# Optimization experiments

Hardware: AMD Instinct MI355X
Metric: run time of the kernel (lower is better)

## Reference

```python
import jax, jax.numpy as jnp
import numpy as np

N_NODES = 128   # input_series_dim (nodes per graph)
FEAT = 512      # input_series_length
HID = 512       # hidden_channels
OUT = 10        # output_dimension
BATCH = 512     # batch_size


def setup_inputs() -> dict:
    key = jax.random.key(0)
    ks = jax.random.split(key, 9)
    s = 0.02
    x = jax.random.normal(ks[0], (BATCH, N_NODES, FEAT), jnp.float32)
    # dense_to_sparse(ones(N_NODES, N_NODES)) -> fully connected incl. diagonal,
    # row-major order, covering only nodes 0..N_NODES-1 (faithful to source).
    r = jnp.repeat(jnp.arange(N_NODES, dtype=jnp.int32), N_NODES)
    c = jnp.tile(jnp.arange(N_NODES, dtype=jnp.int32), N_NODES)
    edge_index = jnp.stack([r, c])  # (2, N_NODES**2)
    batch = jnp.repeat(jnp.arange(BATCH, dtype=jnp.int32), N_NODES)  # (BATCH*N_NODES,)
    W1 = jax.random.normal(ks[1], (FEAT, HID), jnp.float32) * s
    b1 = jnp.zeros((HID,), jnp.float32)
    W2 = jax.random.normal(ks[2], (HID, HID), jnp.float32) * s
    b2 = jnp.zeros((HID,), jnp.float32)
    W3 = jax.random.normal(ks[3], (HID, HID), jnp.float32) * s
    b3 = jnp.zeros((HID,), jnp.float32)
    Wlin = jax.random.normal(ks[4], (HID, OUT), jnp.float32) * s
    blin = jnp.zeros((OUT,), jnp.float32)
    return {"x": x, "W1": W1, "b1": b1, "W2": W2, "b2": b2, "W3": W3,
            "b3": b3, "Wlin": Wlin, "blin": blin,
            "edge_index": edge_index, "batch": batch}


def gcn_conv(h, src, dst, W, b):
    # PyG GCNConv: linear transform, add self-loops for ALL N nodes, symmetric norm,
    # scatter-add aggregate at dst, add bias.
    N = h.shape[0]
    h = h @ W
    loop = jnp.arange(N, dtype=src.dtype)
    s = jnp.concatenate([src, loop])
    d = jnp.concatenate([dst, loop])
    deg = jax.ops.segment_sum(jnp.ones(s.shape[0], h.dtype), d, num_segments=N)
    dinv = jnp.where(deg > 0, jax.lax.rsqrt(deg), jnp.zeros((), h.dtype))
    norm = dinv[s] * dinv[d]                     # (E+N,)
    out = jax.ops.segment_sum(norm[:, None] * h[s], d, num_segments=N)
    return out + b


def reference(x, W1, b1, W2, b2, W3, b3, Wlin, blin, edge_index, batch):
    x = x.reshape(-1, x.shape[-1]).astype(jnp.float32)   # (B*N_NODES, FEAT)
    src, dst = edge_index[0], edge_index[1]
    h = jax.nn.relu(gcn_conv(x, src, dst, W1, b1))
    h = jax.nn.relu(gcn_conv(h, src, dst, W2, b2))
    h = gcn_conv(h, src, dst, W3, b3)                    # layers == 3 path
    B = BATCH
    sums = jax.ops.segment_sum(h, batch, num_segments=B)
    cnt = jax.ops.segment_sum(jnp.ones((h.shape[0],), h.dtype), batch, num_segments=B)
    pooled = sums / cnt[:, None]                         # global_mean_pool
    # dropout p=0.5 is identity in eval mode
    return pooled @ Wlin + blin                          # (BATCH, OUT)
```

## Files before the change

kernel.cpp:

```cpp
#include <hip/hip_runtime.h>
#include <hip/hip_bf16.h>


typedef __attribute__((ext_vector_type(8))) short short8;
typedef __attribute__((ext_vector_type(4))) float f32x4;
typedef __attribute__((ext_vector_type(2))) unsigned int uint2v;

#define AS_G __attribute__((address_space(1)))
#define AS_L __attribute__((address_space(3)))

__device__ __forceinline__ void gload_lds16(const void* g, void* l) {
  __builtin_amdgcn_global_load_lds((const AS_G void*)g, (AS_L void*)l, 16, 0, 0);
}

__device__ __forceinline__ unsigned int pack2_bf16(float a, float b) {
  unsigned int ua = __float_as_uint(a);
  unsigned int ub = __float_as_uint(b);
  ua += 0x7FFFu + ((ua >> 16) & 1u);
  ub += 0x7FFFu + ((ub >> 16) & 1u);
  return (ua >> 16) | (ub & 0xFFFF0000u);
}

__device__ __forceinline__ unsigned short bf16_rne(float a) {
  unsigned int ua = __float_as_uint(a);
  ua += 0x7FFFu + ((ua >> 16) & 1u);
  return (unsigned short)(ua >> 16);
}


__global__ __launch_bounds__(1024) void gemm1_f32a(
    const float* __restrict__ A,
    const __hip_bfloat16* __restrict__ Bt,
    const float* __restrict__ bias,
    unsigned short* __restrict__ H,
    float* __restrict__ g0)
{
  __shared__ __align__(16) __hip_bfloat16 smem[40960];

  const int t  = threadIdx.x;
  const int bm = blockIdx.x;
  const int m0 = bm * 128;

  const int wave = t >> 6;
  const int l    = t & 63;
  const int q    = l >> 4;
  const int r16  = l & 15;
  const int wm   = (wave & 1) * 64;
  const int wn   = (wave >> 1) * 64;

  const int brow = t >> 2;
  const int bgc  = (t & 3) ^ ((brow >> 1) & 3);
  const __hip_bfloat16* gb0 = Bt + (size_t)brow * 512 + bgc * 8;
  const __hip_bfloat16* gb1 = gb0 + (size_t)256 * 512;
  __hip_bfloat16* lB0 = smem + wave * 512;
  __hip_bfloat16* lB1 = smem + 8192 + wave * 512;

  const int arow = t >> 3;
  const int kq   = t & 7;
  const float* ga = A + (size_t)(m0 + arow) * 512 + kq * 4;
  const int ac    = (kq >> 1) ^ ((arow >> 1) & 3);
  const int awoff = arow * 32 + ac * 8 + (kq & 1) * 4;

  f32x4 acc[4][4];
#pragma unroll
  for (int i = 0; i < 4; ++i)
#pragma unroll
    for (int j = 0; j < 4; ++j)
      acc[i][j] = (f32x4)0.0f;

  {
    f32x4 a0 = *(const f32x4*)(const void*)ga;
    gload_lds16(gb0, lB0);
    gload_lds16(gb1, lB1);
    uint2v w;
    w[0] = pack2_bf16(a0[0], a0[1]);
    w[1] = pack2_bf16(a0[2], a0[3]);
    *(uint2v*)(void*)(smem + 32768 + awoff) = w;
  }

  for (int kt = 0; kt < 16; ++kt) {
    const int cur = kt & 1;
    const int nxt = cur ^ 1;
    __syncthreads();

    f32x4 aN;
    if (kt < 15) {
      const int ko = (kt + 1) * 32;
      aN = *(const f32x4*)(const void*)(ga + ko);
      gload_lds16(gb0 + ko, smem + nxt * 16384 + wave * 512);
      gload_lds16(gb1 + ko, smem + nxt * 16384 + 8192 + wave * 512);
    }

    short8 af[4], bfr[4];
#pragma unroll
    for (int i = 0; i < 4; ++i) {
      const int row = wm + i * 16 + r16;
      const int c   = (q ^ ((row >> 1) & 3)) << 3;
      af[i] = *(const short8*)(const void*)(smem + 32768 + cur * 4096 + row * 32 + c);
    }
#pragma unroll
    for (int j = 0; j < 4; ++j) {
      const int row = wn + j * 16 + r16;
      const int c   = (q ^ ((row >> 1) & 3)) << 3;
      bfr[j] = *(const short8*)(const void*)(smem + cur * 16384 + row * 32 + c);
    }

#pragma unroll
    for (int i = 0; i < 4; ++i)
#pragma unroll
      for (int j = 0; j < 4; ++j)
        acc[i][j] = __builtin_amdgcn_mfma_f32_16x16x32_bf16(af[i], bfr[j], acc[i][j], 0, 0, 0);

    if (kt < 15) {
      uint2v w;
      w[0] = pack2_bf16(aN[0], aN[1]);
      w[1] = pack2_bf16(aN[2], aN[3]);
      *(uint2v*)(void*)(smem + 32768 + nxt * 4096 + awoff) = w;
    }
  }

  if (bm == 0) {
#pragma unroll
    for (int i = 0; i < 4; ++i)
#pragma unroll
      for (int j = 0; j < 4; ++j) {
        const int col = wn + j * 16 + r16;
#pragma unroll
        for (int r = 0; r < 4; ++r)
          g0[(wm + i * 16 + q * 4 + r) * 512 + col] = acc[i][j][r];
      }
    return;
  }
#pragma unroll
  for (int j = 0; j < 4; ++j) {
    const int col = wn + j * 16 + r16;
    const float bv = bias[col];
#pragma unroll
    for (int i = 0; i < 4; ++i)
#pragma unroll
      for (int r = 0; r < 4; ++r) {
        const int row = m0 + wm + i * 16 + q * 4 + r;
        const float v = fmaxf(acc[i][j][r] + bv, 0.0f);
        const float o = __shfl_xor(v, 1, 64);
        if ((r16 & 1) == 0)
          *(unsigned int*)(void*)(H + (size_t)row * 512 + col) = pack2_bf16(v, o);
      }
  }
}

__global__ __launch_bounds__(1024) void gemm2_pool(
    const __hip_bfloat16* __restrict__ A,
    const __hip_bfloat16* __restrict__ Bt,
    const float* __restrict__ bias,
    float* __restrict__ g0,
    float* __restrict__ P)
{
  __shared__ __align__(16) __hip_bfloat16 smem[40960];

  const int t  = threadIdx.x;
  const int bm = blockIdx.x;
  const int m0 = bm * 128;

  const int wave = t >> 6;
  const int l    = t & 63;
  const int q    = l >> 4;
  const int r16  = l & 15;
  const int wm   = (wave & 1) * 64;
  const int wn   = (wave >> 1) * 64;

  const int brow = t >> 2;
  const int bgc  = (t & 3) ^ ((brow >> 1) & 3);
  const __hip_bfloat16* gb0 = Bt + (size_t)brow * 512 + bgc * 8;
  const __hip_bfloat16* gb1 = gb0 + (size_t)256 * 512;
  __hip_bfloat16* lB0 = smem + wave * 512;
  __hip_bfloat16* lB1 = smem + 8192 + wave * 512;

  const __hip_bfloat16* ga = A + (size_t)(m0 + brow) * 512 + bgc * 8;
  __hip_bfloat16* lA = smem + 32768 + wave * 512;

  f32x4 acc[4][4];
#pragma unroll
  for (int i = 0; i < 4; ++i)
#pragma unroll
    for (int j = 0; j < 4; ++j)
      acc[i][j] = (f32x4)0.0f;

  if (t < 512) gload_lds16(ga, lA);
  gload_lds16(gb0, lB0);
  gload_lds16(gb1, lB1);

  for (int kt = 0; kt < 16; ++kt) {
    const int cur = kt & 1;
    const int nxt = cur ^ 1;
    __syncthreads();

    if (kt < 15) {
      const int ko = (kt + 1) * 32;
      if (t < 512) gload_lds16(ga + ko, smem + 32768 + nxt * 4096 + wave * 512);
      gload_lds16(gb0 + ko, smem + nxt * 16384 + wave * 512);
      gload_lds16(gb1 + ko, smem + nxt * 16384 + 8192 + wave * 512);
    }

    short8 af[4], bfr[4];
#pragma unroll
    for (int i = 0; i < 4; ++i) {
      const int row = wm + i * 16 + r16;
      const int c   = (q ^ ((row >> 1) & 3)) << 3;
      af[i] = *(const short8*)(const void*)(smem + 32768 + cur * 4096 + row * 32 + c);
    }
#pragma unroll
    for (int j = 0; j < 4; ++j) {
      const int row = wn + j * 16 + r16;
      const int c   = (q ^ ((row >> 1) & 3)) << 3;
      bfr[j] = *(const short8*)(const void*)(smem + cur * 16384 + row * 32 + c);
    }

#pragma unroll
    for (int i = 0; i < 4; ++i)
#pragma unroll
      for (int j = 0; j < 4; ++j)
        acc[i][j] = __builtin_amdgcn_mfma_f32_16x16x32_bf16(af[i], bfr[j], acc[i][j], 0, 0, 0);
  }

  __syncthreads();
  float* red = (float*)(smem + 32768);

  if (bm == 0) {
#pragma unroll
    for (int i = 0; i < 4; ++i)
#pragma unroll
      for (int j = 0; j < 4; ++j) {
        const int col = wn + j * 16 + r16;
#pragma unroll
        for (int r = 0; r < 4; ++r)
          g0[(wm + i * 16 + q * 4 + r) * 512 + col] = acc[i][j][r];
      }
    return;
  }

  float s[4];
#pragma unroll
  for (int j = 0; j < 4; ++j) {
    const float bv = bias[wn + j * 16 + r16];
    float a = 0.0f;
#pragma unroll
    for (int i = 0; i < 4; ++i)
#pragma unroll
      for (int r = 0; r < 4; ++r)
        a += fmaxf(acc[i][j][r] + bv, 0.0f);
    a += __shfl_xor(a, 16, 64);
    a += __shfl_xor(a, 32, 64);
    s[j] = a;
  }
  if (q == 0) {
#pragma unroll
    for (int j = 0; j < 4; ++j) red[wave * 64 + j * 16 + r16] = s[j];
  }
  __syncthreads();
  if (t < 512) {
    const int band = t >> 6;
    const int c = t & 63;
    P[(size_t)bm * 512 + band * 64 + c] =
        (red[2 * band * 64 + c] + red[(2 * band + 1) * 64 + c]) * (1.0f / 128.0f);
  }
}

__global__ void fixup_g0_h(const float* __restrict__ g0,
                           const float* __restrict__ bias,
                           unsigned short* __restrict__ H) {
  const int c = blockIdx.x * 128 + threadIdx.x;
  float S = 0.0f;
  for (int i = 0; i < 128; ++i) S += g0[i * 512 + c];
  const float bv = bias[c];
  for (int i = 0; i < 128; ++i) {
    const float v = (S + g0[i * 512 + c]) * (1.0f / 129.0f) + bv;
    H[i * 512 + c] = bf16_rne(fmaxf(v, 0.0f));
  }
}

__global__ void fixup_g0_pool(const float* __restrict__ g0,
                              const float* __restrict__ bias,
                              float* __restrict__ P) {
  const int c = blockIdx.x * 128 + threadIdx.x;
  float S = 0.0f;
  for (int i = 0; i < 128; ++i) S += g0[i * 512 + c];
  const float bv = bias[c];
  float ps = 0.0f;
  for (int i = 0; i < 128; ++i)
    ps += fmaxf((S + g0[i * 512 + c]) * (1.0f / 129.0f) + bv, 0.0f);
  P[c] = ps * (1.0f / 128.0f);
}

__global__ void fold_w(const float* __restrict__ W3,
                       const float* __restrict__ Wlin,
                       const float* __restrict__ b3,
                       const float* __restrict__ blin,
                       float* __restrict__ Wf, float* __restrict__ bfv) {
  const int c = blockIdx.x;
  const int l = threadIdx.x;
  float acc[10];
#pragma unroll
  for (int o = 0; o < 10; ++o) acc[o] = 0.0f;
  for (int n = l; n < 512; n += 64) {
    const float wv = W3[c * 512 + n];
#pragma unroll
    for (int o = 0; o < 10; ++o) acc[o] += wv * Wlin[n * 10 + o];
  }
#pragma unroll
  for (int off = 32; off; off >>= 1)
#pragma unroll
    for (int o = 0; o < 10; ++o) acc[o] += __shfl_down(acc[o], off, 64);
  if (l == 0) {
#pragma unroll
    for (int o = 0; o < 10; ++o) Wf[c * 10 + o] = acc[o];
  }
  if (c < 10) {
    float s = 0.0f;
    for (int k = l; k < 512; k += 64) s += b3[k] * Wlin[k * 10 + c];
#pragma unroll
    for (int off = 32; off; off >>= 1) s += __shfl_down(s, off, 64);
    if (l == 0) bfv[c] = s + blin[c];
  }
}

__global__ void final_out(const float* __restrict__ P,
                          const float* __restrict__ Wf,
                          const float* __restrict__ bfv,
                          float* __restrict__ out) {
  const int m = blockIdx.x;
  const int l = threadIdx.x;
  float acc[10];
#pragma unroll
  for (int o = 0; o < 10; ++o) acc[o] = 0.0f;
  for (int c = l; c < 512; c += 64) {
    const float p = P[m * 512 + c];
#pragma unroll
    for (int o = 0; o < 10; ++o) acc[o] += p * Wf[c * 10 + o];
  }
#pragma unroll
  for (int off = 32; off; off >>= 1)
#pragma unroll
    for (int o = 0; o < 10; ++o) acc[o] += __shfl_down(acc[o], off, 64);
  if (l == 0) {
#pragma unroll
    for (int o = 0; o < 10; ++o) out[m * 10 + o] = acc[o] + bfv[o];
  }
}

__global__ void transpose512x2(const float* __restrict__ Wa,
                               const float* __restrict__ Wb,
                               unsigned short* __restrict__ Wat,
                               unsigned short* __restrict__ Wbt) {
  const float* W = blockIdx.z ? Wb : Wa;
  unsigned short* Wt = blockIdx.z ? Wbt : Wat;
  __shared__ float tile[32][33];
  const int tx = threadIdx.x, ty = threadIdx.y;
  tile[ty][tx] = W[(blockIdx.y * 32 + ty) * 512 + blockIdx.x * 32 + tx];
  __syncthreads();
  Wt[(blockIdx.x * 32 + ty) * 512 + blockIdx.y * 32 + tx] = bf16_rne(tile[tx][ty]);
}

extern "C" void kernel_launch(void* const* d_in, const int* in_sizes, int n_in,
                              void* d_out, int out_size, void* d_ws, size_t ws_size,
                              hipStream_t stream) {
  const float* x    = (const float*)d_in[0];
  const float* W1   = (const float*)d_in[1];
  const float* b1   = (const float*)d_in[2];
  const float* W2   = (const float*)d_in[3];
  const float* b2   = (const float*)d_in[4];
  const float* W3   = (const float*)d_in[5];
  const float* b3   = (const float*)d_in[6];
  const float* Wlin = (const float*)d_in[7];
  const float* blin = (const float*)d_in[8];
  float* out = (float*)d_out;

  char* ws = (char*)d_ws;
  const size_t MB = (size_t)1 << 20;
  unsigned short* H1  = (unsigned short*)ws;
  float* g0           = (float*)(ws + 64 * MB);
  float* P            = (float*)(ws + 64 * MB + 256 * 1024);
  unsigned short* W1t = (unsigned short*)(ws + 65 * MB + 256 * 1024);
  unsigned short* W2t = W1t + 512 * 512;
  float* Wf           = (float*)(W2t + 512 * 512);
  float* bfv          = Wf + 512 * 10;

  transpose512x2<<<dim3(16, 16, 2), dim3(32, 32), 0, stream>>>(W1, W2, W1t, W2t);
  fold_w<<<512, 64, 0, stream>>>(W3, Wlin, b3, blin, Wf, bfv);

  gemm1_f32a<<<512, 1024, 0, stream>>>(
      x, (const __hip_bfloat16*)W1t, b1, H1, g0);
  fixup_g0_h<<<4, 128, 0, stream>>>(g0, b1, H1);

  gemm2_pool<<<512, 1024, 0, stream>>>(
      (const __hip_bfloat16*)H1, (const __hip_bfloat16*)W2t, b2, g0, P);
  fixup_g0_pool<<<4, 128, 0, stream>>>(g0, b2, P);

  final_out<<<512, 64, 0, stream>>>(P, Wf, bfv, out);
}
```

Measured before the change: 331.7 us.

## Fuse both GCN GEMM layers per graph keeping hidden activations in LDS

Merges the first and second GEMM kernels into one kernel per 128-node block. The bf16 hidden activations stay in a swizzled 128x512 LDS tile instead of round-tripping through a global H buffer, and the graph-0 fixups are done in-block via an LDS column reduction, which removes two small fixup launches. This saves about 64 MB of global traffic and two launches. In exchange LDS use doubles to 160 KB, and the second GEMM loads W2 single-buffered with two barriers per k-step, so it loses load/compute overlap.

```diff
diff --git a/kernel.cpp b/kernel.cpp
--- a/kernel.cpp
+++ b/kernel.cpp
@@ -27,20 +27,18 @@
   return (unsigned short)(ua >> 16);
 }
 
-
-__global__ __launch_bounds__(1024) void gemm1_f32a(
-    const float* __restrict__ A,
-    const __hip_bfloat16* __restrict__ Bt,
-    const float* __restrict__ bias,
-    unsigned short* __restrict__ H,
-    float* __restrict__ g0)
+__global__ __launch_bounds__(1024) void fused_gcn(
+    const float* __restrict__ x,
+    const __hip_bfloat16* __restrict__ W1t,
+    const __hip_bfloat16* __restrict__ W2t,
+    const float* __restrict__ b1,
+    const float* __restrict__ b2,
+    float* __restrict__ P)
 {
-  __shared__ __align__(16) __hip_bfloat16 smem[40960];
+  __shared__ __align__(16) __hip_bfloat16 smem[81920];
 
   const int t  = threadIdx.x;
-  const int bm = blockIdx.x;
-  const int m0 = bm * 128;
-
+  const int g  = blockIdx.x;
   const int wave = t >> 6;
   const int l    = t & 63;
   const int q    = l >> 4;
@@ -48,18 +46,16 @@
   const int wm   = (wave & 1) * 64;
   const int wn   = (wave >> 1) * 64;
 
+  const int arow = t >> 3;
+  const int kq   = t & 7;
+  const float* ga = x + ((size_t)g * 128 + arow) * 512 + kq * 4;
+  const int awoff = arow * 32 + (((kq >> 1) ^ ((arow >> 1) & 3)) << 3) + (kq & 1) * 4;
+
   const int brow = t >> 2;
   const int bgc  = (t & 3) ^ ((brow >> 1) & 3);
-  const __hip_bfloat16* gb0 = Bt + (size_t)brow * 512 + bgc * 8;
-  const __hip_bfloat16* gb1 = gb0 + (size_t)256 * 512;
-  __hip_bfloat16* lB0 = smem + wave * 512;
-  __hip_bfloat16* lB1 = smem + 8192 + wave * 512;
-
-  const int arow = t >> 3;
-  const int kq   = t & 7;
-  const float* ga = A + (size_t)(m0 + arow) * 512 + kq * 4;
-  const int ac    = (kq >> 1) ^ ((arow >> 1) & 3);
-  const int awoff = arow * 32 + ac * 8 + (kq & 1) * 4;
+  const size_t boff = (size_t)brow * 512 + bgc * 8;
+  const __hip_bfloat16* g1b0 = W1t + boff;
+  const __hip_bfloat16* g1b1 = g1b0 + (size_t)256 * 512;
 
   f32x4 acc[4][4];
 #pragma unroll
@@ -70,14 +66,13 @@
 
   {
     f32x4 a0 = *(const f32x4*)(const void*)ga;
-    gload_lds16(gb0, lB0);
-    gload_lds16(gb1, lB1);
+    gload_lds16(g1b0, smem + 49152 + wave * 512);
+    gload_lds16(g1b1, smem + 49152 + 8192 + wave * 512);
     uint2v w;
     w[0] = pack2_bf16(a0[0], a0[1]);
     w[1] = pack2_bf16(a0[2], a0[3]);
-    *(uint2v*)(void*)(smem + 32768 + awoff) = w;
-  }
-
+    *(uint2v*)(void*)(smem + awoff) = w;
+  }
   for (int kt = 0; kt < 16; ++kt) {
     const int cur = kt & 1;
     const int nxt = cur ^ 1;
@@ -87,8 +82,8 @@
     if (kt < 15) {
       const int ko = (kt + 1) * 32;
       aN = *(const f32x4*)(const void*)(ga + ko);
-      gload_lds16(gb0 + ko, smem + nxt * 16384 + wave * 512);
-      gload_lds16(gb1 + ko, smem + nxt * 16384 + 8192 + wave * 512);
+      gload_lds16(g1b0 + ko, smem + 49152 + nxt * 16384 + wave * 512);
+      gload_lds16(g1b1 + ko, smem + 49152 + nxt * 16384 + 8192 + wave * 512);
     }
 
     short8 af[4], bfr[4];
@@ -96,15 +91,14 @@
     for (int i = 0; i < 4; ++i) {
       const int row = wm + i * 16 + r16;
       const int c   = (q ^ ((row >> 1) & 3)) << 3;
-      af[i] = *(const short8*)(const void*)(smem + 32768 + cur * 4096 + row * 32 + c);
+      af[i] = *(const short8*)(const void*)(smem + cur * 4096 + row * 32 + c);
     }
 #pragma unroll
     for (int j = 0; j < 4; ++j) {
       const int row = wn + j * 16 + r16;
       const int c   = (q ^ ((row >> 1) & 3)) << 3;
-      bfr[j] = *(const short8*)(const void*)(smem + cur * 16384 + row * 32 + c);
-    }
-
+      bfr[j] = *(const short8*)(const void*)(smem + 49152 + cur * 16384 + row * 32 + c);
+    }
 #pragma unroll
     for (int i = 0; i < 4; ++i)
 #pragma unroll
@@ -115,180 +109,174 @@
       uint2v w;
       w[0] = pack2_bf16(aN[0], aN[1]);
       w[1] = pack2_bf16(aN[2], aN[3]);
-      *(uint2v*)(void*)(smem + 32768 + nxt * 4096 + awoff) = w;
-    }
-  }
-
-  if (bm == 0) {
-#pragma unroll
-    for (int i = 0; i < 4; ++i)
-#pragma unroll
-      for (int j = 0; j < 4; ++j) {
-        const int col = wn + j * 16 + r16;
+      *(uint2v*)(void*)(smem + nxt * 4096 + awoff) = w;
+    }
+  }
+  __syncthreads();
+
+  float* redf = (float*)(smem + 65536);
+  float* Sbuf = (float*)(smem + 67584);
+
+  if (g == 0) {
+    float sj[4];
+#pragma unroll
+    for (int j = 0; j < 4; ++j) {
+      float a = 0.0f;
+#pragma unroll
+      for (int i = 0; i < 4; ++i)
 #pragma unroll
         for (int r = 0; r < 4; ++r)
-          g0[(wm + i * 16 + q * 4 + r) * 512 + col] = acc[i][j][r];
-      }
-    return;
-  }
-#pragma unroll
-  for (int j = 0; j < 4; ++j) {
-    const int col = wn + j * 16 + r16;
-    const float bv = bias[col];
-#pragma unroll
-    for (int i = 0; i < 4; ++i)
-#pragma unroll
-      for (int r = 0; r < 4; ++r) {
-        const int row = m0 + wm + i * 16 + q * 4 + r;
-        const float v = fmaxf(acc[i][j][r] + bv, 0.0f);
-        const float o = __shfl_xor(v, 1, 64);
-        if ((r16 & 1) == 0)
-          *(unsigned int*)(void*)(H + (size_t)row * 512 + col) = pack2_bf16(v, o);
-      }
-  }
-}
-
-__global__ __launch_bounds__(1024) void gemm2_pool(
-    const __hip_bfloat16* __restrict__ A,
-    const __hip_bfloat16* __restrict__ Bt,
-    const float* __restrict__ bias,
-    float* __restrict__ g0,
-    float* __restrict__ P)
-{
-  __shared__ __align__(16) __hip_bfloat16 smem[40960];
-
-  const int t  = threadIdx.x;
-  const int bm = blockIdx.x;
-  const int m0 = bm * 128;
-
-  const int wave = t >> 6;
-  const int l    = t & 63;
-  const int q    = l >> 4;
-  const int r16  = l & 15;
-  const int wm   = (wave & 1) * 64;
-  const int wn   = (wave >> 1) * 64;
-
-  const int brow = t >> 2;
-  const int bgc  = (t & 3) ^ ((brow >> 1) & 3);
-  const __hip_bfloat16* gb0 = Bt + (size_t)brow * 512 + bgc * 8;
-  const __hip_bfloat16* gb1 = gb0 + (size_t)256 * 512;
-  __hip_bfloat16* lB0 = smem + wave * 512;
-  __hip_bfloat16* lB1 = smem + 8192 + wave * 512;
-
-  const __hip_bfloat16* ga = A + (size_t)(m0 + brow) * 512 + bgc * 8;
-  __hip_bfloat16* lA = smem + 32768 + wave * 512;
-
-  f32x4 acc[4][4];
+          a += acc[i][j][r];
+      a += __shfl_xor(a, 16, 64);
+      a += __shfl_xor(a, 32, 64);
+      sj[j] = a;
+    }
+    if (q == 0) {
+#pragma unroll
+      for (int j = 0; j < 4; ++j) redf[wave * 64 + j * 16 + r16] = sj[j];
+    }
+    __syncthreads();
+    if (t < 512)
+      Sbuf[t] = redf[((t >> 6) * 2) * 64 + (t & 63)] +
+                redf[((t >> 6) * 2 + 1) * 64 + (t & 63)];
+    __syncthreads();
+#pragma unroll
+    for (int j = 0; j < 4; ++j) {
+      const int col = wn + j * 16 + r16;
+      const float bv = b1[col];
+      const float Sv = Sbuf[col];
+#pragma unroll
+      for (int i = 0; i < 4; ++i)
+#pragma unroll
+        for (int r = 0; r < 4; ++r) {
+          const int row = wm + i * 16 + q * 4 + r;
+          const float v = fmaxf((Sv + acc[i][j][r]) * (1.0f / 129.0f) + bv, 0.0f);
+          const float o = __shfl_xor(v, 1, 64);
+          if ((r16 & 1) == 0) {
+            const int sl = (col >> 3) ^ (row & 7);
+            *(unsigned int*)(void*)(smem + row * 512 + sl * 8 + (col & 7)) = pack2_bf16(v, o);
+          }
+        }
+    }
+  } else {
+#pragma unroll
+    for (int j = 0; j < 4; ++j) {
+      const int col = wn + j * 16 + r16;
+      const float bv = b1[col];
+#pragma unroll
+      for (int i = 0; i < 4; ++i)
+#pragma unroll
+        for (int r = 0; r < 4; ++r) {
+          const int row = wm + i * 16 + q * 4 + r;
+          const float v = fmaxf(acc[i][j][r] + bv, 0.0f);
+          const float o = __shfl_xor(v, 1, 64);
+          if ((r16 & 1) == 0) {
+            const int sl = (col >> 3) ^ (row & 7);
+            *(unsigned int*)(void*)(smem + row * 512 + sl * 8 + (col & 7)) = pack2_bf16(v, o);
+          }
+        }
+    }
+  }
+
 #pragma unroll
   for (int i = 0; i < 4; ++i)
 #pragma unroll
     for (int j = 0; j < 4; ++j)
       acc[i][j] = (f32x4)0.0f;
 
-  if (t < 512) gload_lds16(ga, lA);
-  gload_lds16(gb0, lB0);
-  gload_lds16(gb1, lB1);
+  const __hip_bfloat16* g2b0 = W2t + boff;
+  const __hip_bfloat16* g2b1 = g2b0 + (size_t)256 * 512;
 
   for (int kt = 0; kt < 16; ++kt) {
-    const int cur = kt & 1;
-    const int nxt = cur ^ 1;
-    __syncthreads();
-
-    if (kt < 15) {
-      const int ko = (kt + 1) * 32;
-      if (t < 512) gload_lds16(ga + ko, smem + 32768 + nxt * 4096 + wave * 512);
-      gload_lds16(gb0 + ko, smem + nxt * 16384 + wave * 512);
-      gload_lds16(gb1 + ko, smem + nxt * 16384 + 8192 + wave * 512);
-    }
+    __syncthreads();
+    const int ko = kt * 32;
+    gload_lds16(g2b0 + ko, smem + 65536 + wave * 512);
+    gload_lds16(g2b1 + ko, smem + 65536 + 8192 + wave * 512);
+    __syncthreads();
 
     short8 af[4], bfr[4];
 #pragma unroll
     for (int i = 0; i < 4; ++i) {
       const int row = wm + i * 16 + r16;
-      const int c   = (q ^ ((row >> 1) & 3)) << 3;
-      af[i] = *(const short8*)(const void*)(smem + 32768 + cur * 4096 + row * 32 + c);
+      const int sl  = (kt * 4 + q) ^ (row & 7);
+      af[i] = *(const short8*)(const void*)(smem + row * 512 + sl * 8);
     }
 #pragma unroll
     for (int j = 0; j < 4; ++j) {
       const int row = wn + j * 16 + r16;
       const int c   = (q ^ ((row >> 1) & 3)) << 3;
-      bfr[j] = *(const short8*)(const void*)(smem + cur * 16384 + row * 32 + c);
-    }
-
+      bfr[j] = *(const short8*)(const void*)(smem + 65536 + row * 32 + c);
+    }
 #pragma unroll
     for (int i = 0; i < 4; ++i)
 #pragma unroll
       for (int j = 0; j < 4; ++j)
         acc[i][j] = __builtin_amdgcn_mfma_f32_16x16x32_bf16(af[i], bfr[j], acc[i][j], 0, 0, 0);
   }
-
   __syncthreads();
-  float* red = (float*)(smem + 32768);
-
-  if (bm == 0) {
-#pragma unroll
-    for (int i = 0; i < 4; ++i)
-#pragma unroll
-      for (int j = 0; j < 4; ++j) {
-        const int col = wn + j * 16 + r16;
+
+  float pj[4];
+  if (g == 0) {
+    float sj[4];
+#pragma unroll
+    for (int j = 0; j < 4; ++j) {
+      float a = 0.0f;
+#pragma unroll
+      for (int i = 0; i < 4; ++i)
 #pragma unroll
         for (int r = 0; r < 4; ++r)
-          g0[(wm + i * 16 + q * 4 + r) * 512 + col] = acc[i][j][r];
-      }
-    return;
-  }
-
-  float s[4];
-#pragma unroll
-  for (int j = 0; j < 4; ++j) {
-    const float bv = bias[wn + j * 16 + r16];
-    float a = 0.0f;
-#pragma unroll
-    for (int i = 0; i < 4; ++i)
-#pragma unroll
-      for (int r = 0; r < 4; ++r)
-        a += fmaxf(acc[i][j][r] + bv, 0.0f);
-    a += __shfl_xor(a, 16, 64);
-    a += __shfl_xor(a, 32, 64);
-    s[j] = a;
+          a += acc[i][j][r];
+      a += __shfl_xor(a, 16, 64);
+      a += __shfl_xor(a, 32, 64);
+      sj[j] = a;
+    }
+    if (q == 0) {
+#pragma unroll
+      for (int j = 0; j < 4; ++j) redf[wave * 64 + j * 16 + r16] = sj[j];
+    }
+    __syncthreads();
+    if (t < 512)
+      Sbuf[t] = redf[((t >> 6) * 2) * 64 + (t & 63)] +
+                redf[((t >> 6) * 2 + 1) * 64 + (t & 63)];
+    __syncthreads();
+#pragma unroll
+    for (int j = 0; j < 4; ++j) {
+      const float bv = b2[wn + j * 16 + r16];
+      const float Sv = Sbuf[wn + j * 16 + r16];
+      float a = 0.0f;
+#pragma unroll
+      for (int i = 0; i < 4; ++i)
+#pragma unroll
+        for (int r = 0; r < 4; ++r)
+          a += fmaxf((Sv + acc[i][j][r]) * (1.0f / 129.0f) + bv, 0.0f);
+      a += __shfl_xor(a, 16, 64);
+      a += __shfl_xor(a, 32, 64);
+      pj[j] = a;
+    }
+  } else {
+#pragma unroll
+    for (int j = 0; j < 4; ++j) {
+      const float bv = b2[wn + j * 16 + r16];
+      float a = 0.0f;
+#pragma unroll
+      for (int i = 0; i < 4; ++i)
+#pragma unroll
+        for (int r = 0; r < 4; ++r)
+          a += fmaxf(acc[i][j][r] + bv, 0.0f);
+      a += __shfl_xor(a, 16, 64);
+      a += __shfl_xor(a, 32, 64);
+      pj[j] = a;
+    }
   }
   if (q == 0) {
 #pragma unroll
-    for (int j = 0; j < 4; ++j) red[wave * 64 + j * 16 + r16] = s[j];
+    for (int j = 0; j < 4; ++j) redf[wave * 64 + j * 16 + r16] = pj[j];
   }
   __syncthreads();
-  if (t < 512) {
-    const int band = t >> 6;
-    const int c = t & 63;
-    P[(size_t)bm * 512 + band * 64 + c] =
-        (red[2 * band * 64 + c] + red[(2 * band + 1) * 64 + c]) * (1.0f / 128.0f);
-  }
-}
-
-__global__ void fixup_g0_h(const float* __restrict__ g0,
-                           const float* __restrict__ bias,
-                           unsigned short* __restrict__ H) {
-  const int c = blockIdx.x * 128 + threadIdx.x;
-  float S = 0.0f;
-  for (int i = 0; i < 128; ++i) S += g0[i * 512 + c];
-  const float bv = bias[c];
-  for (int i = 0; i < 128; ++i) {
-    const float v = (S + g0[i * 512 + c]) * (1.0f / 129.0f) + bv;
-    H[i * 512 + c] = bf16_rne(fmaxf(v, 0.0f));
-  }
-}
-
-__global__ void fixup_g0_pool(const float* __restrict__ g0,
-                              const float* __restrict__ bias,
-                              float* __restrict__ P) {
-  const int c = blockIdx.x * 128 + threadIdx.x;
-  float S = 0.0f;
-  for (int i = 0; i < 128; ++i) S += g0[i * 512 + c];
-  const float bv = bias[c];
-  float ps = 0.0f;
-  for (int i = 0; i < 128; ++i)
-    ps += fmaxf((S + g0[i * 512 + c]) * (1.0f / 129.0f) + bv, 0.0f);
-  P[c] = ps * (1.0f / 128.0f);
+  if (t < 512)
+    P[(size_t)g * 512 + t] =
+        (redf[((t >> 6) * 2) * 64 + (t & 63)] +
+         redf[((t >> 6) * 2 + 1) * 64 + (t & 63)]) * (1.0f / 128.0f);
 }
 
 __global__ void fold_w(const float* __restrict__ W3,
@@ -375,25 +363,17 @@
   float* out = (float*)d_out;
 
   char* ws = (char*)d_ws;
-  const size_t MB = (size_t)1 << 20;
-  unsigned short* H1  = (unsigned short*)ws;
-  float* g0           = (float*)(ws + 64 * MB);
-  float* P            = (float*)(ws + 64 * MB + 256 * 1024);
-  unsigned short* W1t = (unsigned short*)(ws + 65 * MB + 256 * 1024);
+  unsigned short* W1t = (unsigned short*)ws;
   unsigned short* W2t = W1t + 512 * 512;
-  float* Wf           = (float*)(W2t + 512 * 512);
+  float* P            = (float*)(W2t + 512 * 512);
+  float* Wf           = P + 512 * 512;
   float* bfv          = Wf + 512 * 10;
 
   transpose512x2<<<dim3(16, 16, 2), dim3(32, 32), 0, stream>>>(W1, W2, W1t, W2t);
   fold_w<<<512, 64, 0, stream>>>(W3, Wlin, b3, blin, Wf, bfv);
 
-  gemm1_f32a<<<512, 1024, 0, stream>>>(
-      x, (const __hip_bfloat16*)W1t, b1, H1, g0);
-  fixup_g0_h<<<4, 128, 0, stream>>>(g0, b1, H1);
-
-  gemm2_pool<<<512, 1024, 0, stream>>>(
-      (const __hip_bfloat16*)H1, (const __hip_bfloat16*)W2t, b2, g0, P);
-  fixup_g0_pool<<<4, 128, 0, stream>>>(g0, b2, P);
+  fused_gcn<<<512, 1024, 0, stream>>>(
+      x, (const __hip_bfloat16*)W1t, (const __hip_bfloat16*)W2t, b1, b2, P);
 
   final_out<<<512, 64, 0, stream>>>(P, Wf, bfv, out);
 }
```

New measurement: 287.5 us. -13.3%, faster.
